# Kernel tuning notes

Hardware: AMD Instinct MI355X
Metric: run time of the kernel (lower is better)

## Reference

```python
import jax, jax.numpy as jnp
import numpy as np

B, S, D_IN, D_OUT, H = 4, 2048, 1024, 1024, 16
HD = D_OUT // H  # 64


def setup_inputs() -> dict:
    key = jax.random.key(0)
    ks = jax.random.split(key, 6)
    scale_in = 1.0 / np.sqrt(D_IN)
    scale_out = 1.0 / np.sqrt(D_OUT)
    return {
        "x": jax.random.normal(ks[0], (B, S, D_IN), dtype=jnp.float32),
        "Wq": jax.random.normal(ks[1], (D_IN, D_OUT), dtype=jnp.float32) * scale_in,
        "Wk": jax.random.normal(ks[2], (D_IN, D_OUT), dtype=jnp.float32) * scale_in,
        "Wv": jax.random.normal(ks[3], (D_IN, D_OUT), dtype=jnp.float32) * scale_in,
        "Wo": jax.random.normal(ks[4], (D_OUT, D_OUT), dtype=jnp.float32) * scale_out,
        "bo": jax.random.normal(ks[5], (D_OUT,), dtype=jnp.float32) * 0.01,
    }


def reference(x, Wq, Wk, Wv, Wo, bo):
    b, s, _ = x.shape
    # project and split heads: (b, s, d_out) -> (b, h, s, hd)
    def split(t):
        return t.reshape(b, s, H, HD).transpose(0, 2, 1, 3)
    q = split(x @ Wq)
    k = split(x @ Wk)
    v = split(x @ Wv)
    # scaled causal attention scores (b, h, s, s)
    scores = jnp.einsum('bhqd,bhkd->bhqk', q, k) / jnp.sqrt(jnp.float32(HD))
    causal = jnp.tril(jnp.ones((s, s), dtype=bool))
    scores = jnp.where(causal, scores, -jnp.inf)
    weights = jax.nn.softmax(scores, axis=-1)
    # dropout p=0.0 -> identity (eval mode)
    ctx = jnp.einsum('bhqk,bhkd->bhqd', weights, v)
    ctx = ctx.transpose(0, 2, 1, 3).reshape(b, s, D_OUT)
    return ctx @ Wo + bo
```

## Files before the change

### kernel.cpp

```cpp
#include <hip/hip_runtime.h>
#include <stdint.h>

#define DEVINL __device__ __forceinline__

typedef __attribute__((ext_vector_type(8))) __bf16 bf16x8;
typedef __attribute__((ext_vector_type(4))) float f32x4;
typedef __attribute__((ext_vector_type(8))) unsigned short u16x8;
typedef __attribute__((ext_vector_type(2))) unsigned int u32x2;

constexpr int Bc = 4, Sc = 2048, DINc = 1024, Hc = 16;
constexpr float QSCALE = 0.18033688011112042f;

DEVINL unsigned short f2bf(float x) {
  unsigned u = __builtin_bit_cast(unsigned, x);
  u += 0x7fffu + ((u >> 16) & 1u);
  return (unsigned short)(u >> 16);
}

DEVINL unsigned pack_bf16_trunc(float p0, float p1) {
  return __builtin_amdgcn_perm(__builtin_bit_cast(unsigned, p1),
                               __builtin_bit_cast(unsigned, p0), 0x07060302u);
}

DEVINL void gload_lds16(const void* g, void* l) {
  __builtin_amdgcn_global_load_lds(
      (const __attribute__((address_space(1))) void*)g,
      (__attribute__((address_space(3))) void*)l, 16, 0, 0);
}

template <int ROWS>
DEVINL void stage_tile(const unsigned short* g, int ld, void* lds, int tid) {
#pragma unroll
  for (int p = 0; p < ROWS / 32; ++p) {
    int L = (p * 256 + tid) * 16;
    int row = L >> 7;
    int cb = L & 127;
    int scb = cb ^ ((row & 7) << 4);
    gload_lds16((const char*)(g + (size_t)row * ld) + scb, (char*)lds + L);
  }
}

DEVINL bf16x8 read_frag(const void* lds, int row, int kelem) {
  int addr = row * 128 + (((kelem * 2) ^ ((row & 7) << 4)));
  return *(const bf16x8*)((const char*)lds + addr);
}

__global__ __launch_bounds__(256) void cvt_bf16(const float* __restrict__ in,
                                                unsigned short* __restrict__ out,
                                                int n) {
  int i = (blockIdx.x * 256 + threadIdx.x) * 8;
  if (i + 8 > n) return;
  f32x4 a = *(const f32x4*)(in + i);
  f32x4 b = *(const f32x4*)(in + i + 4);
  u16x8 r;
  r[0] = f2bf(a[0]); r[1] = f2bf(a[1]); r[2] = f2bf(a[2]); r[3] = f2bf(a[3]);
  r[4] = f2bf(b[0]); r[5] = f2bf(b[1]); r[6] = f2bf(b[2]); r[7] = f2bf(b[3]);
  *(u16x8*)(out + i) = r;
}

__global__ __launch_bounds__(256) void transpose_convert(
    const float* __restrict__ src, unsigned short* __restrict__ dst, int K, int N) {
  __shared__ float t[64][65];
  int n0 = blockIdx.x * 64, k0 = blockIdx.y * 64;
  int tx = threadIdx.x & 63, ty = threadIdx.x >> 6;
#pragma unroll
  for (int r = 0; r < 64; r += 4)
    t[r + ty][tx] = src[(size_t)(k0 + r + ty) * N + n0 + tx];
  __syncthreads();
#pragma unroll
  for (int r = 0; r < 64; r += 4)
    dst[(size_t)(n0 + r + ty) * K + k0 + tx] = f2bf(t[tx][r + ty]);
}

__global__ __launch_bounds__(256, 2) void gemm_qkv(
    const unsigned short* __restrict__ A, const unsigned short* __restrict__ Bt,
    unsigned short* __restrict__ qws, unsigned short* __restrict__ kws,
    unsigned short* __restrict__ vtws) {
  __shared__ __align__(16) unsigned short lA[128 * 64];
  __shared__ __align__(16) unsigned short lB[128 * 64];
  int tid = threadIdx.x, lane = tid & 63, wave = tid >> 6;
  int wr = wave >> 1, wc = wave & 1;
  int bm = blockIdx.x, bn = blockIdx.y;
  const unsigned short* Ab = A + (size_t)bm * 128 * 1024;
  const unsigned short* Bb = Bt + (size_t)bn * 128 * 1024;
  int r15 = lane & 15, khi = (lane >> 4) * 8;

  f32x4 acc[4][4];
#pragma unroll
  for (int i = 0; i < 4; ++i)
#pragma unroll
    for (int j = 0; j < 4; ++j) acc[i][j] = (f32x4){0.f, 0.f, 0.f, 0.f};

  for (int k0 = 0; k0 < 1024; k0 += 64) {
    stage_tile<128>(Ab + k0, 1024, lA, tid);
    stage_tile<128>(Bb + k0, 1024, lB, tid);
    __syncthreads();
#pragma unroll
    for (int ks = 0; ks < 2; ++ks) {
      bf16x8 af[4], bfr[4];
#pragma unroll
      for (int i = 0; i < 4; ++i)
        af[i] = read_frag(lA, wr * 64 + i * 16 + r15, ks * 32 + khi);
#pragma unroll
      for (int j = 0; j < 4; ++j)
        bfr[j] = read_frag(lB, wc * 64 + j * 16 + r15, ks * 32 + khi);
#pragma unroll
      for (int i = 0; i < 4; ++i)
#pragma unroll
        for (int j = 0; j < 4; ++j)
          acc[i][j] = __builtin_amdgcn_mfma_f32_16x16x32_bf16(af[i], bfr[j], acc[i][j], 0, 0, 0);
    }
    __syncthreads();
  }

  int sel = bn >> 3;
  int colbase = (bn & 7) * 128 + wc * 64;
  int mbase = bm * 128 + wr * 64;
#pragma unroll
  for (int i = 0; i < 4; ++i) {
#pragma unroll
    for (int r = 0; r < 4; ++r) {
      int m = mbase + i * 16 + (lane >> 4) * 4 + r;
      int b = m >> 11, s = m & 2047;
#pragma unroll
      for (int j = 0; j < 4; ++j) {
        int col = colbase + j * 16 + r15;
        int h = col >> 6, d = col & 63;
        int bh = b * 16 + h;
        if (sel == 0)
          qws[((size_t)bh * 2048 + s) * 64 + d] = f2bf(acc[i][j][r] * QSCALE);
        else if (sel == 1)
          kws[((size_t)bh * 2048 + s) * 64 + d] = f2bf(acc[i][j][r]);
        else
          vtws[((size_t)bh * 64 + d) * 2048 + s] = f2bf(acc[i][j][r]);
      }
    }
  }
}

__global__ __launch_bounds__(256, 3) void attn(
    const unsigned short* __restrict__ qws, const unsigned short* __restrict__ kws,
    const unsigned short* __restrict__ vtws, unsigned short* __restrict__ ctx) {
  __shared__ __align__(16) unsigned short lK[2][64 * 64];
  __shared__ __align__(16) unsigned short lV[2][64 * 64];
  __shared__ __align__(16) unsigned short lP[4][32 * 64];
  int tid = threadIdx.x, lane = tid & 63, wave = tid >> 6;
  int lid = blockIdx.x + 8 * blockIdx.y;
  int bh = (lid & 7) * 8 + ((lid >> 3) & 7);
  int pairid = lid >> 6;
  int r15 = lane & 15, g4 = lane >> 4;
  const unsigned short* Kb = kws + (size_t)bh * 2048 * 64;
  const unsigned short* Vb = vtws + (size_t)bh * 64 * 2048;
  int b = bh >> 4, h = bh & 15;
  char* Pw = (char*)&lP[wave][0];

#pragma unroll 1
  for (int seg = 0; seg < 2; ++seg) {
    int t = seg == 0 ? (15 - pairid) : pairid;
    int q0 = t * 128;
    int myrow0 = q0 + wave * 32;
    const unsigned short* Qb = qws + ((size_t)bh * 2048 + myrow0) * 64;

    bf16x8 qf[2][2];
#pragma unroll
    for (int mf = 0; mf < 2; ++mf)
#pragma unroll
      for (int ks = 0; ks < 2; ++ks)
        qf[mf][ks] = *(const bf16x8*)(Qb + (size_t)(mf * 16 + r15) * 64 + ks * 32 + g4 * 8);

    float m_run[2] = {-1e30f, -1e30f}, l_run[2] = {0.f, 0.f};
    f32x4 o_acc[2][4];
#pragma unroll
    for (int mf = 0; mf < 2; ++mf)
#pragma unroll
      for (int df = 0; df < 4; ++df) o_acc[mf][df] = (f32x4){0.f, 0.f, 0.f, 0.f};

    int nkt = 2 * t + 2;
    __syncthreads();
    int cur = 0;
    stage_tile<64>(Kb, 64, lK[0], tid);
    stage_tile<64>(Vb, 2048, lV[0], tid);

#pragma unroll 1
    for (int kt = 0; kt < nkt; ++kt) {
      __syncthreads();
      if (kt + 1 < nkt) {
        stage_tile<64>(Kb + (size_t)(kt + 1) * 64 * 64, 64, lK[cur ^ 1], tid);
        stage_tile<64>(Vb + (size_t)(kt + 1) * 64, 2048, lV[cur ^ 1], tid);
      }

      f32x4 sacc[2][4];
#pragma unroll
      for (int mf = 0; mf < 2; ++mf)
#pragma unroll
        for (int nf = 0; nf < 4; ++nf) sacc[mf][nf] = (f32x4){0.f, 0.f, 0.f, 0.f};
#pragma unroll
      for (int ks = 0; ks < 2; ++ks) {
        bf16x8 kf[4];
#pragma unroll
        for (int nf = 0; nf < 4; ++nf)
          kf[nf] = read_frag(lK[cur], nf * 16 + r15, ks * 32 + g4 * 8);
        __builtin_amdgcn_s_setprio(1);
#pragma unroll
        for (int mf = 0; mf < 2; ++mf)
#pragma unroll
          for (int nf = 0; nf < 4; ++nf)
            sacc[mf][nf] = __builtin_amdgcn_mfma_f32_16x16x32_bf16(kf[nf], qf[mf][ks], sacc[mf][nf], 0, 0, 0);
        __builtin_amdgcn_s_setprio(0);
      }

      if (kt * 64 + 63 > myrow0) {
#pragma unroll
        for (int mf = 0; mf < 2; ++mf) {
          int q = myrow0 + mf * 16 + r15;
#pragma unroll
          for (int nf = 0; nf < 4; ++nf) {
            int kbase = kt * 64 + nf * 16 + g4 * 4;
#pragma unroll
            for (int r = 0; r < 4; ++r)
              if (kbase + r > q) sacc[mf][nf][r] = -3e38f;
          }
        }
      }

      float tm[2];
#pragma unroll
      for (int mf = 0; mf < 2; ++mf) {
        float a0 = fmaxf(fmaxf(sacc[mf][0][0], sacc[mf][0][1]), fmaxf(sacc[mf][0][2], sacc[mf][0][3]));
        float a1 = fmaxf(fmaxf(sacc[mf][1][0], sacc[mf][1][1]), fmaxf(sacc[mf][1][2], sacc[mf][1][3]));
        float a2 = fmaxf(fmaxf(sacc[mf][2][0], sacc[mf][2][1]), fmaxf(sacc[mf][2][2], sacc[mf][2][3]));
        float a3 = fmaxf(fmaxf(sacc[mf][3][0], sacc[mf][3][1]), fmaxf(sacc[mf][3][2], sacc[mf][3][3]));
        float m = fmaxf(fmaxf(a0, a1), fmaxf(a2, a3));
        m = fmaxf(m, __shfl_xor(m, 16));
        m = fmaxf(m, __shfl_xor(m, 32));
        tm[mf] = m;
      }

      bool ok = (tm[0] <= m_run[0] + 11.5f) & (tm[1] <= m_run[1] + 11.5f);
      if (!__all(ok)) {
#pragma unroll
        for (int mf = 0; mf < 2; ++mf) {
          float mn = fmaxf(m_run[mf], tm[mf]);
          float a = __builtin_amdgcn_exp2f(m_run[mf] - mn);
          m_run[mf] = mn;
          l_run[mf] *= a;
          float av[4];
#pragma unroll
          for (int r = 0; r < 4; ++r)
            av[r] = __shfl(a, (g4 * 4 + r) | (lane & 48));
#pragma unroll
          for (int df = 0; df < 4; ++df)
#pragma unroll
            for (int r = 0; r < 4; ++r) o_acc[mf][df][r] *= av[r];
        }
      }

      float rs[2] = {0.f, 0.f};
#pragma unroll
      for (int mf = 0; mf < 2; ++mf) {
        int prow = mf * 16 + r15;
        char* Prow = Pw + prow * 128;
        int sw = (prow & 7) << 4;
#pragma unroll
        for (int nf = 0; nf < 4; ++nf) {
          float p0 = __builtin_amdgcn_exp2f(sacc[mf][nf][0] - m_run[mf]);
          float p1 = __builtin_amdgcn_exp2f(sacc[mf][nf][1] - m_run[mf]);
          float p2 = __builtin_amdgcn_exp2f(sacc[mf][nf][2] - m_run[mf]);
          float p3 = __builtin_amdgcn_exp2f(sacc[mf][nf][3] - m_run[mf]);
          rs[mf] += (p0 + p1) + (p2 + p3);
          *(u32x2*)(Prow + (((nf * 16 + g4 * 4) * 2) ^ sw)) =
              (u32x2){pack_bf16_trunc(p0, p1), pack_bf16_trunc(p2, p3)};
        }
        float s = rs[mf];
        s += __shfl_xor(s, 16);
        s += __shfl_xor(s, 32);
        l_run[mf] += s;
      }

#pragma unroll
      for (int ks = 0; ks < 2; ++ks) {
        bf16x8 vf[4];
#pragma unroll
        for (int df = 0; df < 4; ++df)
          vf[df] = read_frag(lV[cur], df * 16 + r15, ks * 32 + g4 * 8);
        bf16x8 pf[2];
#pragma unroll
        for (int mf = 0; mf < 2; ++mf)
          pf[mf] = read_frag(Pw, mf * 16 + r15, ks * 32 + g4 * 8);
        __builtin_amdgcn_s_setprio(1);
#pragma unroll
        for (int mf = 0; mf < 2; ++mf)
#pragma unroll
          for (int df = 0; df < 4; ++df)
            o_acc[mf][df] = __builtin_amdgcn_mfma_f32_16x16x32_bf16(pf[mf], vf[df], o_acc[mf][df], 0, 0, 0);
        __builtin_amdgcn_s_setprio(0);
      }
      cur ^= 1;
    }

#pragma unroll
    for (int mf = 0; mf < 2; ++mf) {
      float rl = 1.f / l_run[mf];
      float rv[4];
#pragma unroll
      for (int r = 0; r < 4; ++r)
        rv[r] = __shfl(rl, (g4 * 4 + r) | (lane & 48));
#pragma unroll
      for (int r = 0; r < 4; ++r) {
        int row = myrow0 + mf * 16 + g4 * 4 + r;
#pragma unroll
        for (int df = 0; df < 4; ++df)
          ctx[((size_t)(b * 2048 + row)) * 1024 + h * 64 + df * 16 + r15] =
              f2bf(o_acc[mf][df][r] * rv[r]);
      }
    }
  }
}

__global__ __launch_bounds__(256, 2) void gemm_out(
    const unsigned short* __restrict__ A, const unsigned short* __restrict__ Bt,
    const float* __restrict__ bo, float* __restrict__ out) {
  __shared__ __align__(16) unsigned short lA[128 * 64];
  __shared__ __align__(16) unsigned short lB[128 * 64];
  int tid = threadIdx.x, lane = tid & 63, wave = tid >> 6;
  int wr = wave >> 1, wc = wave & 1;
  int bm = blockIdx.x, bn = blockIdx.y;
  const unsigned short* Ab = A + (size_t)bm * 128 * 1024;
  const unsigned short* Bb = Bt + (size_t)bn * 128 * 1024;
  int r15 = lane & 15, khi = (lane >> 4) * 8;

  f32x4 acc[4][4];
#pragma unroll
  for (int i = 0; i < 4; ++i)
#pragma unroll
    for (int j = 0; j < 4; ++j) acc[i][j] = (f32x4){0.f, 0.f, 0.f, 0.f};

  for (int k0 = 0; k0 < 1024; k0 += 64) {
    stage_tile<128>(Ab + k0, 1024, lA, tid);
    stage_tile<128>(Bb + k0, 1024, lB, tid);
    __syncthreads();
#pragma unroll
    for (int ks = 0; ks < 2; ++ks) {
      bf16x8 af[4], bfr[4];
#pragma unroll
      for (int i = 0; i < 4; ++i)
        af[i] = read_frag(lA, wr * 64 + i * 16 + r15, ks * 32 + khi);
#pragma unroll
      for (int j = 0; j < 4; ++j)
        bfr[j] = read_frag(lB, wc * 64 + j * 16 + r15, ks * 32 + khi);
#pragma unroll
      for (int i = 0; i < 4; ++i)
#pragma unroll
        for (int j = 0; j < 4; ++j)
          acc[i][j] = __builtin_amdgcn_mfma_f32_16x16x32_bf16(af[i], bfr[j], acc[i][j], 0, 0, 0);
    }
    __syncthreads();
  }

  int nbase = bn * 128 + wc * 64;
  int mbase = bm * 128 + wr * 64;
#pragma unroll
  for (int j = 0; j < 4; ++j) {
    int n = nbase + j * 16 + r15;
    float bias = bo[n];
#pragma unroll
    for (int i = 0; i < 4; ++i)
#pragma unroll
      for (int r = 0; r < 4; ++r) {
        int m = mbase + i * 16 + (lane >> 4) * 4 + r;
        out[(size_t)m * 1024 + n] = acc[i][j][r] + bias;
      }
  }
}

extern "C" void kernel_launch(void* const* d_in, const int* in_sizes, int n_in,
                              void* d_out, int out_size, void* d_ws, size_t ws_size,
                              hipStream_t stream) {
  const float* x = (const float*)d_in[0];
  const float* Wq = (const float*)d_in[1];
  const float* Wk = (const float*)d_in[2];
  const float* Wv = (const float*)d_in[3];
  const float* Wo = (const float*)d_in[4];
  const float* bo = (const float*)d_in[5];
  float* out = (float*)d_out;

  char* ws = (char*)d_ws;
  unsigned short* xb    = (unsigned short*)(ws);
  unsigned short* wqkvt = (unsigned short*)(ws + (16u << 20));
  unsigned short* wot   = (unsigned short*)(ws + (22u << 20));
  unsigned short* qws   = (unsigned short*)(ws + (24u << 20));
  unsigned short* kws   = (unsigned short*)(ws + (40u << 20));
  unsigned short* vtws  = (unsigned short*)(ws + (56u << 20));
  unsigned short* ctxws = (unsigned short*)(ws + (72u << 20));

  cvt_bf16<<<dim3(4096), dim3(256), 0, stream>>>(x, xb, Bc * Sc * DINc);
  transpose_convert<<<dim3(16, 16), dim3(256), 0, stream>>>(Wq, wqkvt, 1024, 1024);
  transpose_convert<<<dim3(16, 16), dim3(256), 0, stream>>>(Wk, wqkvt + (size_t)1024 * 1024, 1024, 1024);
  transpose_convert<<<dim3(16, 16), dim3(256), 0, stream>>>(Wv, wqkvt + (size_t)2048 * 1024, 1024, 1024);
  transpose_convert<<<dim3(16, 16), dim3(256), 0, stream>>>(Wo, wot, 1024, 1024);

  gemm_qkv<<<dim3(64, 24), dim3(256), 0, stream>>>(xb, wqkvt, qws, kws, vtws);
  attn<<<dim3(8, 64), dim3(256), 0, stream>>>(qws, kws, vtws, ctxws);
  gemm_out<<<dim3(64, 8), dim3(256), 0, stream>>>(ctxws, wot, bo, out);
}
```

Baseline: 186.2 us.

## Double-buffer LDS in projection GEMMs and merge weight transposes into one launch

```diff
diff --git a/kernel.cpp b/kernel.cpp
--- a/kernel.cpp
+++ b/kernel.cpp
@@ -58,26 +58,35 @@
   *(u16x8*)(out + i) = r;
 }
 
-__global__ __launch_bounds__(256) void transpose_convert(
-    const float* __restrict__ src, unsigned short* __restrict__ dst, int K, int N) {
+__global__ __launch_bounds__(256) void transpose_convert4(
+    const float* __restrict__ Wq, const float* __restrict__ Wk,
+    const float* __restrict__ Wv, const float* __restrict__ Wo,
+    unsigned short* __restrict__ wqkvt, unsigned short* __restrict__ wot) {
   __shared__ float t[64][65];
+  const float* src;
+  unsigned short* dst;
+  int z = blockIdx.z;
+  if (z == 0)      { src = Wq; dst = wqkvt; }
+  else if (z == 1) { src = Wk; dst = wqkvt + (size_t)1024 * 1024; }
+  else if (z == 2) { src = Wv; dst = wqkvt + (size_t)2048 * 1024; }
+  else             { src = Wo; dst = wot; }
   int n0 = blockIdx.x * 64, k0 = blockIdx.y * 64;
   int tx = threadIdx.x & 63, ty = threadIdx.x >> 6;
 #pragma unroll
   for (int r = 0; r < 64; r += 4)
-    t[r + ty][tx] = src[(size_t)(k0 + r + ty) * N + n0 + tx];
+    t[r + ty][tx] = src[(size_t)(k0 + r + ty) * 1024 + n0 + tx];
   __syncthreads();
 #pragma unroll
   for (int r = 0; r < 64; r += 4)
-    dst[(size_t)(n0 + r + ty) * K + k0 + tx] = f2bf(t[tx][r + ty]);
+    dst[(size_t)(n0 + r + ty) * 1024 + k0 + tx] = f2bf(t[tx][r + ty]);
 }
 
 __global__ __launch_bounds__(256, 2) void gemm_qkv(
     const unsigned short* __restrict__ A, const unsigned short* __restrict__ Bt,
     unsigned short* __restrict__ qws, unsigned short* __restrict__ kws,
     unsigned short* __restrict__ vtws) {
-  __shared__ __align__(16) unsigned short lA[128 * 64];
-  __shared__ __align__(16) unsigned short lB[128 * 64];
+  __shared__ __align__(16) unsigned short lA[2][128 * 64];
+  __shared__ __align__(16) unsigned short lB[2][128 * 64];
   int tid = threadIdx.x, lane = tid & 63, wave = tid >> 6;
   int wr = wave >> 1, wc = wave & 1;
   int bm = blockIdx.x, bn = blockIdx.y;
@@ -91,26 +100,34 @@
 #pragma unroll
     for (int j = 0; j < 4; ++j) acc[i][j] = (f32x4){0.f, 0.f, 0.f, 0.f};
 
-  for (int k0 = 0; k0 < 1024; k0 += 64) {
-    stage_tile<128>(Ab + k0, 1024, lA, tid);
-    stage_tile<128>(Bb + k0, 1024, lB, tid);
+  int cur = 0;
+  stage_tile<128>(Ab, 1024, lA[0], tid);
+  stage_tile<128>(Bb, 1024, lB[0], tid);
+#pragma unroll 1
+  for (int t = 0; t < 16; ++t) {
     __syncthreads();
+    if (t + 1 < 16) {
+      stage_tile<128>(Ab + (t + 1) * 64, 1024, lA[cur ^ 1], tid);
+      stage_tile<128>(Bb + (t + 1) * 64, 1024, lB[cur ^ 1], tid);
+    }
 #pragma unroll
     for (int ks = 0; ks < 2; ++ks) {
       bf16x8 af[4], bfr[4];
 #pragma unroll
       for (int i = 0; i < 4; ++i)
-        af[i] = read_frag(lA, wr * 64 + i * 16 + r15, ks * 32 + khi);
+        af[i] = read_frag(lA[cur], wr * 64 + i * 16 + r15, ks * 32 + khi);
 #pragma unroll
       for (int j = 0; j < 4; ++j)
-        bfr[j] = read_frag(lB, wc * 64 + j * 16 + r15, ks * 32 + khi);
+        bfr[j] = read_frag(lB[cur], wc * 64 + j * 16 + r15, ks * 32 + khi);
+      __builtin_amdgcn_s_setprio(1);
 #pragma unroll
       for (int i = 0; i < 4; ++i)
 #pragma unroll
         for (int j = 0; j < 4; ++j)
           acc[i][j] = __builtin_amdgcn_mfma_f32_16x16x32_bf16(af[i], bfr[j], acc[i][j], 0, 0, 0);
-    }
-    __syncthreads();
+      __builtin_amdgcn_s_setprio(0);
+    }
+    cur ^= 1;
   }
 
   int sel = bn >> 3;
@@ -320,8 +337,8 @@
 __global__ __launch_bounds__(256, 2) void gemm_out(
     const unsigned short* __restrict__ A, const unsigned short* __restrict__ Bt,
     const float* __restrict__ bo, float* __restrict__ out) {
-  __shared__ __align__(16) unsigned short lA[128 * 64];
-  __shared__ __align__(16) unsigned short lB[128 * 64];
+  __shared__ __align__(16) unsigned short lA[2][128 * 64];
+  __shared__ __align__(16) unsigned short lB[2][128 * 64];
   int tid = threadIdx.x, lane = tid & 63, wave = tid >> 6;
   int wr = wave >> 1, wc = wave & 1;
   int bm = blockIdx.x, bn = blockIdx.y;
@@ -335,26 +352,34 @@
 #pragma unroll
     for (int j = 0; j < 4; ++j) acc[i][j] = (f32x4){0.f, 0.f, 0.f, 0.f};
 
-  for (int k0 = 0; k0 < 1024; k0 += 64) {
-    stage_tile<128>(Ab + k0, 1024, lA, tid);
-    stage_tile<128>(Bb + k0, 1024, lB, tid);
+  int cur = 0;
+  stage_tile<128>(Ab, 1024, lA[0], tid);
+  stage_tile<128>(Bb, 1024, lB[0], tid);
+#pragma unroll 1
+  for (int t = 0; t < 16; ++t) {
     __syncthreads();
+    if (t + 1 < 16) {
+      stage_tile<128>(Ab + (t + 1) * 64, 1024, lA[cur ^ 1], tid);
+      stage_tile<128>(Bb + (t + 1) * 64, 1024, lB[cur ^ 1], tid);
+    }
 #pragma unroll
     for (int ks = 0; ks < 2; ++ks) {
       bf16x8 af[4], bfr[4];
 #pragma unroll
       for (int i = 0; i < 4; ++i)
-        af[i] = read_frag(lA, wr * 64 + i * 16 + r15, ks * 32 + khi);
+        af[i] = read_frag(lA[cur], wr * 64 + i * 16 + r15, ks * 32 + khi);
 #pragma unroll
       for (int j = 0; j < 4; ++j)
-        bfr[j] = read_frag(lB, wc * 64 + j * 16 + r15, ks * 32 + khi);
+        bfr[j] = read_frag(lB[cur], wc * 64 + j * 16 + r15, ks * 32 + khi);
+      __builtin_amdgcn_s_setprio(1);
 #pragma unroll
       for (int i = 0; i < 4; ++i)
 #pragma unroll
         for (int j = 0; j < 4; ++j)
           acc[i][j] = __builtin_amdgcn_mfma_f32_16x16x32_bf16(af[i], bfr[j], acc[i][j], 0, 0, 0);
-    }
-    __syncthreads();
+      __builtin_amdgcn_s_setprio(0);
+    }
+    cur ^= 1;
   }
 
   int nbase = bn * 128 + wc * 64;
@@ -394,10 +419,7 @@
   unsigned short* ctxws = (unsigned short*)(ws + (72u << 20));
 
   cvt_bf16<<<dim3(4096), dim3(256), 0, stream>>>(x, xb, Bc * Sc * DINc);
-  transpose_convert<<<dim3(16, 16), dim3(256), 0, stream>>>(Wq, wqkvt, 1024, 1024);
-  transpose_convert<<<dim3(16, 16), dim3(256), 0, stream>>>(Wk, wqkvt + (size_t)1024 * 1024, 1024, 1024);
-  transpose_convert<<<dim3(16, 16), dim3(256), 0, stream>>>(Wv, wqkvt + (size_t)2048 * 1024, 1024, 1024);
-  transpose_convert<<<dim3(16, 16), dim3(256), 0, stream>>>(Wo, wot, 1024, 1024);
+  transpose_convert4<<<dim3(16, 16, 4), dim3(256), 0, stream>>>(Wq, Wk, Wv, Wo, wqkvt, wot);
 
   gemm_qkv<<<dim3(64, 24), dim3(256), 0, stream>>>(xb, wqkvt, qws, kws, vtws);
   attn<<<dim3(8, 64), dim3(256), 0, stream>>>(qws, kws, vtws, ctxws);
```

After: 177.0 us. 4.9% less time.
